# Kernel optimization log

Hardware: AMD Instinct MI355X
Metric: run time of the kernel (lower is better)

Reference implementation:

```python
import jax, jax.numpy as jnp
import numpy as np

EPS = 1e-6
B, I, N, Wd, R = 128, 512, 512, 32, 4


def setup_inputs() -> dict:
    key = jax.random.key(0)
    ks = jax.random.split(key, 32)
    inp = {
        "xi": jax.random.normal(ks[0], (B, I), jnp.float32),
        "memory": jax.random.normal(ks[1], (B, N, Wd), jnp.float32),
        "link_matrix": jax.random.uniform(ks[2], (B, N, N), jnp.float32),
        "precedence": jax.random.uniform(ks[3], (B, N), jnp.float32),
        "read_weights": jax.random.uniform(ks[4], (B, R, N), jnp.float32),
        "write_weights": jax.random.uniform(ks[5], (B, N), jnp.float32),
        "usage": jax.random.uniform(ks[6], (B, N), jnp.float32),
    }
    # 10 independent linear heads (weight [out, in], bias [out]) as in independent_linears=True
    dims = [("rk", R * Wd), ("rs", R), ("wk", Wd), ("ws", 1), ("ev", Wd),
            ("wv", Wd), ("fg", R), ("ag", 1), ("wg", 1), ("rm", 3 * R)]
    scale = 1.0 / np.sqrt(I).astype(np.float32)
    for i, (nm, d) in enumerate(dims):
        inp["W_" + nm] = jax.random.normal(ks[7 + 2 * i], (d, I), jnp.float32) * scale
        inp["b_" + nm] = jax.random.normal(ks[8 + 2 * i], (d,), jnp.float32) * 0.01
    return inp


def reference(xi, memory, link_matrix, precedence, read_weights, write_weights, usage,
              W_rk, b_rk, W_rs, b_rs, W_wk, b_wk, W_ws, b_ws, W_ev, b_ev,
              W_wv, b_wv, W_fg, b_fg, W_ag, b_ag, W_wg, b_wg, W_rm, b_rm):
    b, n, w = memory.shape
    r = b_rs.shape[0]
    lin = lambda Wm, bm: xi @ Wm.T + bm

    # interface vectors
    read_keys = jnp.tanh(lin(W_rk, b_rk)).reshape(b, r, w)          # [B,R,W]
    read_str = jax.nn.softplus(lin(W_rs, b_rs))                      # [B,R]
    write_key = jnp.tanh(lin(W_wk, b_wk))                            # [B,W]
    write_str = jax.nn.softplus(lin(W_ws, b_ws))                     # [B,1]
    erase = jax.nn.sigmoid(lin(W_ev, b_ev))                          # [B,W]
    write_vec = jnp.tanh(lin(W_wv, b_wv))                            # [B,W]
    free = jax.nn.sigmoid(lin(W_fg, b_fg))                           # [B,R]
    alloc_g = jax.nn.sigmoid(lin(W_ag, b_ag))                        # [B,1]
    write_g = jax.nn.sigmoid(lin(W_wg, b_wg))                        # [B,1]
    modes = jax.nn.softmax(lin(W_rm, b_rm).reshape(b, r, 3), axis=2)

    # usage update (memory retention)
    psi = jnp.prod(1.0 - free[:, :, None] * read_weights, axis=1)    # [B,N]
    usage = (usage + write_weights - usage * write_weights) * psi

    # allocation weighting via sorted usage
    idx = jnp.argsort(usage, axis=1)
    su = jnp.take_along_axis(usage, idx, axis=1)
    prod_excl = jnp.concatenate(
        [jnp.ones((b, 1), su.dtype), jnp.cumprod(su, axis=1)[:, :-1]], axis=1)
    alloc_sorted = (1.0 - su) * prod_excl
    alloc = jnp.zeros_like(usage).at[jnp.arange(b)[:, None], idx].set(alloc_sorted)

    # write content addressing (cosine similarity)
    mem_norm = jnp.linalg.norm(memory, axis=2)                       # [B,N]
    wsim = jnp.einsum('bnw,bw->bn', memory, write_key) / (
        mem_norm * jnp.linalg.norm(write_key, axis=1, keepdims=True) + EPS)
    wc = jax.nn.softmax(write_str * wsim, axis=1)                    # [B,N]

    ww = write_g * (alloc_g * alloc + (1.0 - alloc_g) * wc)          # [B,N]

    # memory write (erase then add)
    memory = memory * (1.0 - ww[:, :, None] * erase[:, None, :]) \
             + ww[:, :, None] * write_vec[:, None, :]

    # temporal link matrix + precedence update
    link = (1.0 - ww[:, :, None] - ww[:, None, :]) * link_matrix \
           + ww[:, :, None] * precedence[:, None, :]
    link = link * (1.0 - jnp.eye(n, dtype=link.dtype))
    precedence = (1.0 - jnp.sum(ww, axis=1, keepdims=True)) * precedence + ww

    # directional read weights from previous read weights
    fw = jnp.einsum('bnm,brm->brn', link, read_weights)              # forward: L w
    bw = jnp.einsum('bmn,brm->brn', link, read_weights)              # backward: L^T w

    # read content addressing on updated memory
    mem_norm2 = jnp.linalg.norm(memory, axis=2)
    rsim = jnp.einsum('bnw,brw->brn', memory, read_keys) / (
        mem_norm2[:, None, :] * jnp.linalg.norm(read_keys, axis=2, keepdims=True) + EPS)
    rc = jax.nn.softmax(read_str[:, :, None] * rsim, axis=2)         # [B,R,N]

    read_weights = modes[:, :, 0:1] * bw + modes[:, :, 1:2] * rc + modes[:, :, 2:3] * fw
    read_vectors = jnp.einsum('brn,bnw->brw', read_weights, memory)  # [B,R,W]
    return read_vectors, memory, link, precedence, read_weights, ww, usage
```

## Files before the change

kernel.cpp:

```cpp
#include <hip/hip_runtime.h>
#include <math.h>

#define BB 128
#define ID 512
#define NN 512
#define WDIM 32
#define RR 4
#define EPSF 1e-6f
#define NTILE 16

typedef float nt_float4 __attribute__((ext_vector_type(4)));

#define OFF_RV   ((size_t)0)
#define OFF_MEM  (OFF_RV + (size_t)BB*RR*WDIM)
#define OFF_LINK (OFF_MEM + (size_t)BB*NN*WDIM)
#define OFF_PREC (OFF_LINK + (size_t)BB*NN*NN)
#define OFF_RW   (OFF_PREC + (size_t)BB*NN)
#define OFF_WW   (OFF_RW + (size_t)BB*RR*NN)
#define OFF_USG  (OFF_WW + (size_t)BB*NN)

#define IF_RK 0
#define IF_RS 128
#define IF_WK 132
#define IF_WS 164
#define IF_EV 165
#define IF_WV 197
#define IF_FG 229
#define IF_AG 233
#define IF_WG 234
#define IF_RM 235

#define WS_IFACE ((size_t)0)
#define WS_FW    (WS_IFACE + (size_t)BB*256)
#define WS_BW    (WS_FW + (size_t)BB*RR*NN)
#define WS_PART  WS_BW
#define WS_PART_FLOATS ((size_t)BB*NTILE*RR*NN)

__device__ __forceinline__ float sigm(float x) { return 1.0f / (1.0f + expf(-x)); }
__device__ __forceinline__ float softplusf(float x) { return fmaxf(x, 0.0f) + log1pf(expf(-fabsf(x))); }

struct HeadArgs {
  const float *Wrk, *brk, *Wrs, *brs, *Wwk, *bwk, *Wws, *bws, *Wev, *bev,
              *Wwv, *bwv, *Wfg, *bfg, *Wag, *bag, *Wwg, *bwg, *Wrm, *brm;
};

__global__ __launch_bounds__(256) void k1_heads(const float* __restrict__ xi, HeadArgs ha,
                                                float* __restrict__ iface) {
  __shared__ __align__(16) float xs[ID];
  __shared__ float raw[256];
  int b = blockIdx.x, t = threadIdx.x;
  for (int i = t; i < ID; i += 256) xs[i] = xi[b * ID + i];
  __syncthreads();
  const float* Ws[10] = {ha.Wrk, ha.Wrs, ha.Wwk, ha.Wws, ha.Wev, ha.Wwv, ha.Wfg, ha.Wag, ha.Wwg, ha.Wrm};
  const float* bs[10] = {ha.brk, ha.brs, ha.bwk, ha.bws, ha.bev, ha.bwv, ha.bfg, ha.bag, ha.bwg, ha.brm};
  const int off[11] = {0, 128, 132, 164, 165, 197, 229, 233, 234, 235, 247};
  float val = 0.0f;
  int h = -1, row = 0;
  if (t < 247) {
    for (int k = 0; k < 10; ++k)
      if (t >= off[k] && t < off[k + 1]) { h = k; row = t - off[k]; }
    const float4* w4 = (const float4*)(Ws[h] + row * ID);
    const float4* x4 = (const float4*)xs;
    float acc = 0.0f;
    for (int i = 0; i < ID / 4; ++i) {
      float4 w = w4[i], x = x4[i];
      acc += w.x * x.x + w.y * x.y + w.z * x.z + w.w * x.w;
    }
    val = acc + bs[h][row];
  }
  raw[t] = val;
  __syncthreads();
  if (t < 247) {
    float o;
    if (h == 0 || h == 2 || h == 5) o = tanhf(val);
    else if (h == 1 || h == 3) o = softplusf(val);
    else if (h == 9) {
      int g = (t - 235) / 3;
      float a0 = raw[235 + g * 3], a1 = raw[236 + g * 3], a2 = raw[237 + g * 3];
      float mx = fmaxf(a0, fmaxf(a1, a2));
      o = expf(val - mx) / (expf(a0 - mx) + expf(a1 - mx) + expf(a2 - mx));
    } else o = sigm(val);
    iface[b * 256 + t] = o;
  }
}

__global__ __launch_bounds__(512) void k2_write(const float* __restrict__ mem_in,
                                                const float* __restrict__ prec_in,
                                                const float* __restrict__ rw_in,
                                                const float* __restrict__ wwt_in,
                                                const float* __restrict__ usg_in,
                                                const float* __restrict__ iface,
                                                float* __restrict__ bw,
                                                float* __restrict__ out) {
  __shared__ __align__(16) float sif[256];
  __shared__ float sv[NN];
  __shared__ int si[NN];
  __shared__ float salloc[NN];
  __shared__ float sred[8];
  __shared__ float swt[8];
  int b = blockIdx.x, tid = threadIdx.x;
  int lane = tid & 63, wave = tid >> 6;

  for (int i = tid; i < RR * NN; i += 512) bw[(size_t)b * RR * NN + i] = 0.0f;

  if (tid < 256) sif[tid] = iface[b * 256 + tid];
  __syncthreads();

  const float* rwb = rw_in + (size_t)b * RR * NN;
  float psi = 1.0f;
#pragma unroll
  for (int r = 0; r < RR; r++) psi *= 1.0f - sif[IF_FG + r] * rwb[r * NN + tid];
  float u = usg_in[b * NN + tid], wwt = wwt_in[b * NN + tid];
  u = (u + wwt - u * wwt) * psi;

  float v = u; int idx = tid;
  for (int k = 2; k <= NN; k <<= 1) {
    for (int j = k >> 1; j > 0; j >>= 1) {
      int p = tid ^ j;
      float pv; int pi;
      if (j >= 64) {
        sv[tid] = v; si[tid] = idx;
        __syncthreads();
        pv = sv[p]; pi = si[p];
        __syncthreads();
      } else {
        pv = __shfl_xor(v, j);
        pi = __shfl_xor(idx, j);
      }
      bool mineSmaller = (v < pv) || (v == pv && idx < pi);
      bool keepMin = (((tid & k) == 0) == (tid < p));
      bool take = keepMin ? !mineSmaller : mineSmaller;
      if (take) { v = pv; idx = pi; }
    }
  }

  float pr = v;
#pragma unroll
  for (int o = 1; o < 64; o <<= 1) {
    float q = __shfl_up(pr, o);
    if (lane >= o) pr *= q;
  }
  if (lane == 63) swt[wave] = pr;
  __syncthreads();
  float wp = 1.0f;
#pragma unroll
  for (int w = 0; w < 8; w++) if (w < wave) wp *= swt[w];
  float ep = __shfl_up(pr, 1);
  if (lane == 0) ep = 1.0f;
  float alloc_sorted = (1.0f - v) * (wp * ep);
  salloc[idx] = alloc_sorted;
  __syncthreads();
  float alloc = salloc[tid];

  const float4* mrow = (const float4*)(mem_in + ((size_t)b * NN + tid) * WDIM);
  float4 mv[8];
  float dot = 0, nrm = 0, wkn = 0;
#pragma unroll
  for (int i = 0; i < 8; i++) {
    float4 m = mrow[i];
    mv[i] = m;
    const float4 kk = *(const float4*)&sif[IF_WK + 4 * i];
    dot += m.x * kk.x + m.y * kk.y + m.z * kk.z + m.w * kk.w;
    nrm += m.x * m.x + m.y * m.y + m.z * m.z + m.w * m.w;
    wkn += kk.x * kk.x + kk.y * kk.y + kk.z * kk.z + kk.w * kk.w;
  }
  float s = sif[IF_WS] * (dot / (sqrtf(nrm) * sqrtf(wkn) + EPSF));

  float m8 = s;
#pragma unroll
  for (int d = 32; d > 0; d >>= 1) m8 = fmaxf(m8, __shfl_down(m8, d));
  if (lane == 0) sred[wave] = m8;
  __syncthreads();
  float mx = sred[0];
#pragma unroll
  for (int w = 1; w < 8; w++) mx = fmaxf(mx, sred[w]);
  __syncthreads();
  float e = expf(s - mx);
  float sm = e;
#pragma unroll
  for (int d = 32; d > 0; d >>= 1) sm += __shfl_down(sm, d);
  if (lane == 0) sred[wave] = sm;
  __syncthreads();
  float esum = 0;
#pragma unroll
  for (int w = 0; w < 8; w++) esum += sred[w];
  __syncthreads();
  float wc = e / esum;

  float ww = sif[IF_WG] * (sif[IF_AG] * alloc + (1.0f - sif[IF_AG]) * wc);
  out[OFF_WW + b * NN + tid] = ww;
  out[OFF_USG + b * NN + tid] = u;

  float ws_ = ww;
#pragma unroll
  for (int d = 32; d > 0; d >>= 1) ws_ += __shfl_down(ws_, d);
  if (lane == 0) sred[wave] = ws_;
  __syncthreads();
  float wsum = 0;
#pragma unroll
  for (int w = 0; w < 8; w++) wsum += sred[w];
  out[OFF_PREC + b * NN + tid] = (1.0f - wsum) * prec_in[b * NN + tid] + ww;

  float* mo = out + OFF_MEM + ((size_t)b * NN + tid) * WDIM;
#pragma unroll
  for (int i = 0; i < 8; i++) {
    float4 m = mv[i];
    float4 o;
    o.x = m.x * (1.0f - ww * sif[IF_EV + 4 * i + 0]) + ww * sif[IF_WV + 4 * i + 0];
    o.y = m.y * (1.0f - ww * sif[IF_EV + 4 * i + 1]) + ww * sif[IF_WV + 4 * i + 1];
    o.z = m.z * (1.0f - ww * sif[IF_EV + 4 * i + 2]) + ww * sif[IF_WV + 4 * i + 2];
    o.w = m.w * (1.0f - ww * sif[IF_EV + 4 * i + 3]) + ww * sif[IF_WV + 4 * i + 3];
    ((float4*)mo)[i] = o;
  }
}

template<int PARTIAL>
__global__ __launch_bounds__(256) void k3_link(const float* __restrict__ link_in,
                                               const float* __restrict__ prec_in,
                                               const float* __restrict__ rw_in,
                                               const float* __restrict__ ww_out,
                                               float* __restrict__ link_out,
                                               float* __restrict__ fw,
                                               float* __restrict__ bw) {
  __shared__ __align__(16) float sww[NN];
  __shared__ __align__(16) float sprec[NN];
  __shared__ __align__(16) float srw[RR * NN];
  __shared__ float sbw[RR * NN];
  int b = blockIdx.y, tile = blockIdx.x, tid = threadIdx.x;
  for (int i = tid; i < NN; i += 256) {
    sww[i] = ww_out[b * NN + i];
    sprec[i] = prec_in[b * NN + i];
  }
  for (int i = tid; i < RR * NN; i += 256) {
    srw[i] = rw_in[(size_t)b * RR * NN + i];
    sbw[i] = 0.0f;
  }
  __syncthreads();

  int wave = tid >> 6, lane = tid & 63;
  float4 cww[2], cpr[2], crw[RR][2];
#pragma unroll
  for (int h = 0; h < 2; h++) {
    cww[h] = ((const float4*)sww)[h * 64 + lane];
    cpr[h] = ((const float4*)sprec)[h * 64 + lane];
#pragma unroll
    for (int r = 0; r < RR; r++) crw[r][h] = ((const float4*)(srw + r * NN))[h * 64 + lane];
  }

  float bwa[RR][8];
#pragma unroll
  for (int r = 0; r < RR; r++)
#pragma unroll
    for (int j = 0; j < 8; j++) bwa[r][j] = 0.0f;

  const size_t lbase = (size_t)b * NN * NN;
  const float* lbp = link_in + lbase;
  int row0 = tile * 32 + wave;

  float4 na0 = ((const float4*)(lbp + (size_t)row0 * NN))[lane];
  float4 na1 = ((const float4*)(lbp + (size_t)row0 * NN))[64 + lane];
  float4 nb0 = ((const float4*)(lbp + (size_t)(row0 + 4) * NN))[lane];
  float4 nb1 = ((const float4*)(lbp + (size_t)(row0 + 4) * NN))[64 + lane];

  for (int i = 0; i < 8; i++) {
    int row = row0 + 4 * i;
    float4 cv[2];
    if ((i & 1) == 0) { cv[0] = na0; cv[1] = na1; } else { cv[0] = nb0; cv[1] = nb1; }
    if (i < 6) {
      const float4* Ln = (const float4*)(lbp + (size_t)(row + 8) * NN);
      if ((i & 1) == 0) { na0 = Ln[lane]; na1 = Ln[64 + lane]; }
      else              { nb0 = Ln[lane]; nb1 = Ln[64 + lane]; }
    }
    float wwr = sww[row];
    float rwr[RR] = {srw[row], srw[NN + row], srw[2 * NN + row], srw[3 * NN + row]};
    nt_float4* Lo = (nt_float4*)(link_out + lbase + (size_t)row * NN);
    float fp[RR] = {0, 0, 0, 0};
#pragma unroll
    for (int h = 0; h < 2; h++) {
      float4 lv = cv[h];
      float l[4] = {lv.x, lv.y, lv.z, lv.w};
      float wc[4] = {cww[h].x, cww[h].y, cww[h].z, cww[h].w};
      float pc[4] = {cpr[h].x, cpr[h].y, cpr[h].z, cpr[h].w};
      int c0 = h * 256 + 4 * lane;
#pragma unroll
      for (int j = 0; j < 4; j++) {
        float ln = (1.0f - wwr - wc[j]) * l[j] + wwr * pc[j];
        if (c0 + j == row) ln = 0.0f;
        l[j] = ln;
#pragma unroll
        for (int r = 0; r < RR; r++) bwa[r][h * 4 + j] += ln * rwr[r];
      }
#pragma unroll
      for (int r = 0; r < RR; r++) {
        float rc0 = (r == 0) ? crw[0][h].x : (r == 1) ? crw[1][h].x : (r == 2) ? crw[2][h].x : crw[3][h].x;
        float rc1 = (r == 0) ? crw[0][h].y : (r == 1) ? crw[1][h].y : (r == 2) ? crw[2][h].y : crw[3][h].y;
        float rc2 = (r == 0) ? crw[0][h].z : (r == 1) ? crw[1][h].z : (r == 2) ? crw[2][h].z : crw[3][h].z;
        float rc3 = (r == 0) ? crw[0][h].w : (r == 1) ? crw[1][h].w : (r == 2) ? crw[2][h].w : crw[3][h].w;
        fp[r] += l[0] * rc0 + l[1] * rc1 + l[2] * rc2 + l[3] * rc3;
      }
      nt_float4 ov = {l[0], l[1], l[2], l[3]};
      __builtin_nontemporal_store(ov, &Lo[h * 64 + lane]);
    }
#pragma unroll
    for (int d = 32; d > 0; d >>= 1) {
      fp[0] += __shfl_down(fp[0], d);
      fp[1] += __shfl_down(fp[1], d);
      fp[2] += __shfl_down(fp[2], d);
      fp[3] += __shfl_down(fp[3], d);
    }
    if (lane == 0) {
      float* fwb = fw + (size_t)b * RR * NN;
      fwb[0 * NN + row] = fp[0];
      fwb[1 * NN + row] = fp[1];
      fwb[2 * NN + row] = fp[2];
      fwb[3 * NN + row] = fp[3];
    }
  }

  for (int w = 0; w < 4; w++) {
    if (wave == w) {
#pragma unroll
      for (int r = 0; r < RR; r++)
#pragma unroll
        for (int h = 0; h < 2; h++)
#pragma unroll
          for (int j = 0; j < 4; j++)
            sbw[r * NN + h * 256 + 4 * lane + j] += bwa[r][h * 4 + j];
    }
    __syncthreads();
  }
  if (PARTIAL) {
    float* bp = bw + ((size_t)(b * NTILE + tile)) * RR * NN;
    for (int i = tid; i < RR * NN; i += 256) bp[i] = sbw[i];
  } else {
    float* bp = bw + (size_t)b * RR * NN;
    for (int i = tid; i < RR * NN; i += 256) atomicAdd(&bp[i], sbw[i]);
  }
}

template<int PARTIAL>
__global__ __launch_bounds__(512) void k4_read(const float* __restrict__ iface,
                                               const float* __restrict__ fw,
                                               const float* __restrict__ bw,
                                               float* __restrict__ out) {
  __shared__ __align__(16) float srk[WDIM];
  __shared__ float sred[8];
  __shared__ float srwn[NN];
  __shared__ float spart[16][WDIM];
  int b = blockIdx.x >> 2, r = blockIdx.x & 3;
  int tid = threadIdx.x, lane = tid & 63, wave = tid >> 6;
  const float* ifb = iface + b * 256;
  if (tid < WDIM) srk[tid] = ifb[IF_RK + r * WDIM + tid];
  __syncthreads();
  float rkn2 = 0;
#pragma unroll
  for (int w = 0; w < WDIM; w++) { float v = srk[w]; rkn2 += v * v; }
  float rkn = sqrtf(rkn2);

  const float* mem = out + OFF_MEM + (size_t)b * NN * WDIM;
  const float4* mrow = (const float4*)(mem + (size_t)tid * WDIM);
  float d = 0, nrm = 0;
#pragma unroll
  for (int i = 0; i < 8; i++) {
    float4 m = mrow[i];
    const float4 kk = *(const float4*)&srk[4 * i];
    nrm += m.x * m.x + m.y * m.y + m.z * m.z + m.w * m.w;
    d += m.x * kk.x + m.y * kk.y + m.z * kk.z + m.w * kk.w;
  }
  float s = ifb[IF_RS + r] * (d / (sqrtf(nrm) * rkn + EPSF));

  float m8 = s;
#pragma unroll
  for (int dd = 32; dd > 0; dd >>= 1) m8 = fmaxf(m8, __shfl_down(m8, dd));
  if (lane == 0) sred[wave] = m8;
  __syncthreads();
  float mx = sred[0];
#pragma unroll
  for (int w = 1; w < 8; w++) mx = fmaxf(mx, sred[w]);
  __syncthreads();
  float e = expf(s - mx);
  float sm = e;
#pragma unroll
  for (int dd = 32; dd > 0; dd >>= 1) sm += __shfl_down(sm, dd);
  if (lane == 0) sred[wave] = sm;
  __syncthreads();
  float esum = 0;
#pragma unroll
  for (int w = 0; w < 8; w++) esum += sred[w];
  float rc = e / esum;

  float bwv;
  if (PARTIAL) {
    const float* pp = bw + ((size_t)b * NTILE * RR + r) * NN + tid;
    float acc = 0.0f;
#pragma unroll
    for (int t = 0; t < NTILE; t++) acc += pp[(size_t)t * RR * NN];
    bwv = acc;
  } else {
    bwv = bw[((size_t)b * RR + r) * NN + tid];
  }
  float fwv = fw[((size_t)b * RR + r) * NN + tid];
  float m0 = ifb[IF_RM + 3 * r], m1 = ifb[IF_RM + 3 * r + 1], m2 = ifb[IF_RM + 3 * r + 2];
  float v = m0 * bwv + m1 * rc + m2 * fwv;
  srwn[tid] = v;
  out[OFF_RW + ((size_t)b * RR + r) * NN + tid] = v;
  __syncthreads();

  int w = tid & 31, part = tid >> 5;
  float acc = 0;
  const float* mp = mem + (size_t)part * 32 * WDIM + w;
  const float* rp = srwn + part * 32;
#pragma unroll
  for (int n = 0; n < 32; n++) acc += rp[n] * mp[(size_t)n * WDIM];
  spart[part][w] = acc;
  __syncthreads();
  if (tid < WDIM) {
    float vv = 0;
#pragma unroll
    for (int p = 0; p < 16; p++) vv += spart[p][tid];
    out[OFF_RV + ((size_t)b * RR + r) * WDIM + tid] = vv;
  }
}

extern "C" void kernel_launch(void* const* d_in, const int* in_sizes, int n_in,
                              void* d_out, int out_size, void* d_ws, size_t ws_size,
                              hipStream_t stream) {
  const float* xi = (const float*)d_in[0];
  const float* mem = (const float*)d_in[1];
  const float* link = (const float*)d_in[2];
  const float* prec = (const float*)d_in[3];
  const float* rw = (const float*)d_in[4];
  const float* wwt = (const float*)d_in[5];
  const float* usg = (const float*)d_in[6];
  HeadArgs ha;
  ha.Wrk = (const float*)d_in[7];  ha.brk = (const float*)d_in[8];
  ha.Wrs = (const float*)d_in[9];  ha.brs = (const float*)d_in[10];
  ha.Wwk = (const float*)d_in[11]; ha.bwk = (const float*)d_in[12];
  ha.Wws = (const float*)d_in[13]; ha.bws = (const float*)d_in[14];
  ha.Wev = (const float*)d_in[15]; ha.bev = (const float*)d_in[16];
  ha.Wwv = (const float*)d_in[17]; ha.bwv = (const float*)d_in[18];
  ha.Wfg = (const float*)d_in[19]; ha.bfg = (const float*)d_in[20];
  ha.Wag = (const float*)d_in[21]; ha.bag = (const float*)d_in[22];
  ha.Wwg = (const float*)d_in[23]; ha.bwg = (const float*)d_in[24];
  ha.Wrm = (const float*)d_in[25]; ha.brm = (const float*)d_in[26];

  float* out = (float*)d_out;
  float* ws = (float*)d_ws;
  float* iface = ws + WS_IFACE;
  float* fwbuf = ws + WS_FW;
  float* bwbuf = ws + WS_BW;

  const size_t need_part_bytes = (WS_PART + WS_PART_FLOATS) * sizeof(float);
  const bool use_partial = ws_size >= need_part_bytes;

  k1_heads<<<BB, 256, 0, stream>>>(xi, ha, iface);
  k2_write<<<BB, 512, 0, stream>>>(mem, prec, rw, wwt, usg, iface, bwbuf, out);
  if (use_partial) {
    k3_link<1><<<dim3(NTILE, BB), 256, 0, stream>>>(link, prec, rw, out + OFF_WW, out + OFF_LINK, fwbuf, ws + WS_PART);
    k4_read<1><<<BB * RR, 512, 0, stream>>>(iface, fwbuf, ws + WS_PART, out);
  } else {
    k3_link<0><<<dim3(NTILE, BB), 256, 0, stream>>>(link, prec, rw, out + OFF_WW, out + OFF_LINK, fwbuf, bwbuf);
    k4_read<0><<<BB * RR, 512, 0, stream>>>(iface, fwbuf, bwbuf, out);
  }
}
```

Baseline: 351.1 us.

## Replace bitonic sort with rank-based product for allocation weights

```diff
diff --git a/kernel.cpp b/kernel.cpp
--- a/kernel.cpp
+++ b/kernel.cpp
@@ -93,11 +93,8 @@
                                                 float* __restrict__ bw,
                                                 float* __restrict__ out) {
   __shared__ __align__(16) float sif[256];
-  __shared__ float sv[NN];
-  __shared__ int si[NN];
-  __shared__ float salloc[NN];
+  __shared__ __align__(16) float su[NN];
   __shared__ float sred[8];
-  __shared__ float swt[8];
   int b = blockIdx.x, tid = threadIdx.x;
   int lane = tid & 63, wave = tid >> 6;
 
@@ -113,44 +110,19 @@
   float u = usg_in[b * NN + tid], wwt = wwt_in[b * NN + tid];
   u = (u + wwt - u * wwt) * psi;
 
-  float v = u; int idx = tid;
-  for (int k = 2; k <= NN; k <<= 1) {
-    for (int j = k >> 1; j > 0; j >>= 1) {
-      int p = tid ^ j;
-      float pv; int pi;
-      if (j >= 64) {
-        sv[tid] = v; si[tid] = idx;
-        __syncthreads();
-        pv = sv[p]; pi = si[p];
-        __syncthreads();
-      } else {
-        pv = __shfl_xor(v, j);
-        pi = __shfl_xor(idx, j);
-      }
-      bool mineSmaller = (v < pv) || (v == pv && idx < pi);
-      bool keepMin = (((tid & k) == 0) == (tid < p));
-      bool take = keepMin ? !mineSmaller : mineSmaller;
-      if (take) { v = pv; idx = pi; }
-    }
-  }
-
-  float pr = v;
-#pragma unroll
-  for (int o = 1; o < 64; o <<= 1) {
-    float q = __shfl_up(pr, o);
-    if (lane >= o) pr *= q;
-  }
-  if (lane == 63) swt[wave] = pr;
-  __syncthreads();
-  float wp = 1.0f;
-#pragma unroll
-  for (int w = 0; w < 8; w++) if (w < wave) wp *= swt[w];
-  float ep = __shfl_up(pr, 1);
-  if (lane == 0) ep = 1.0f;
-  float alloc_sorted = (1.0f - v) * (wp * ep);
-  salloc[idx] = alloc_sorted;
-  __syncthreads();
-  float alloc = salloc[tid];
+  su[tid] = u;
+  __syncthreads();
+
+  float pr0 = 1.0f, pr1 = 1.0f, pr2 = 1.0f, pr3 = 1.0f;
+#pragma unroll 4
+  for (int j = 0; j < NN; j += 4) {
+    float4 uu = *(const float4*)&su[j];
+    pr0 *= ((uu.x < u) || (uu.x == u && (j + 0) < tid)) ? uu.x : 1.0f;
+    pr1 *= ((uu.y < u) || (uu.y == u && (j + 1) < tid)) ? uu.y : 1.0f;
+    pr2 *= ((uu.z < u) || (uu.z == u && (j + 2) < tid)) ? uu.z : 1.0f;
+    pr3 *= ((uu.w < u) || (uu.w == u && (j + 3) < tid)) ? uu.w : 1.0f;
+  }
+  float alloc = (1.0f - u) * ((pr0 * pr1) * (pr2 * pr3));
 
   const float4* mrow = (const float4*)(mem_in + ((size_t)b * NN + tid) * WDIM);
   float4 mv[8];
```

New measurement: 373.5 us. +6.4%, slower.
